# Kernel tuning notes

Hardware: AMD Instinct MI355X
Metric: run time of the kernel (lower is better)

The kernel has to match this reference:

```python
import jax, jax.numpy as jnp
import numpy as np

B, T, C = 4, 2048, 1024   # batch, seq (block_size), n_embd
H, D = 16, 64             # num_heads, head_size (H*D == C)


def setup_inputs() -> dict:
    key = jax.random.key(0)
    ks = jax.random.split(key, 6)
    s = 0.02
    return {
        "x":  jax.random.normal(ks[0], (B, T, C), jnp.float32),
        "Wq": jax.random.normal(ks[1], (H, C, D), jnp.float32) * s,
        "Wk": jax.random.normal(ks[2], (H, C, D), jnp.float32) * s,
        "Wv": jax.random.normal(ks[3], (H, C, D), jnp.float32) * s,
        "Wp": jax.random.normal(ks[4], (C, C), jnp.float32) * s,
        "bp": jnp.zeros((C,), jnp.float32),
        "is_masked": 1,
    }


def reference(x, Wq, Wk, Wv, Wp, bp, is_masked):
    # Batched per-head projections (original loops over H separate Linears)
    q = jnp.einsum("btc,hcd->bhtd", x, Wq)
    k = jnp.einsum("btc,hcd->bhtd", x, Wk)
    v = jnp.einsum("btc,hcd->bhtd", x, Wv)
    # NOTE: original divides by sqrt(C) where C = n_embd (input dim), not head_size
    scores = jnp.einsum("bhtd,bhsd->bhts", q, k) / jnp.sqrt(jnp.asarray(C, x.dtype))
    if is_masked:
        causal = jnp.tril(jnp.ones((T, T), bool))
        scores = jnp.where(causal, scores, jnp.asarray(-jnp.inf, scores.dtype))
    attn = jax.nn.softmax(scores, axis=-1)   # dropout is identity in eval mode
    out = jnp.einsum("bhts,bhsd->bhtd", attn, v)
    # concat heads along the last dim: [B,T,H*D] == [B,T,C]
    out = out.transpose(0, 2, 1, 3).reshape(B, T, C)
    return out @ Wp.T + bp
```

## Files before the change

### kernel.cpp

```cpp
#include <hip/hip_runtime.h>
#include <stdint.h>
#include <type_traits>

typedef unsigned short u16;
typedef unsigned int u32;
typedef __attribute__((ext_vector_type(8))) short frag8;
typedef __attribute__((ext_vector_type(4))) float fx4;
typedef __attribute__((ext_vector_type(16))) float fx16;

#define MFMA(a, b, c) __builtin_amdgcn_mfma_f32_16x16x32_bf16((a), (b), (c), 0, 0, 0)
#define MFMA32(a, b, c) __builtin_amdgcn_mfma_f32_32x32x16_bf16((a), (b), (c), 0, 0, 0)

__device__ __forceinline__ void gload16(const void* g, void* l) {
  __builtin_amdgcn_global_load_lds((const __attribute__((address_space(1))) void*)g,
                                   (__attribute__((address_space(3))) void*)l, 16, 0, 0);
}

__device__ __forceinline__ u16 f2bf(float f) {
  union { float f; unsigned int u; } c; c.f = f;
  unsigned int r = c.u + 0x7FFFu + ((c.u >> 16) & 1u);
  return (u16)(r >> 16);
}

__device__ __forceinline__ u32 cvtpk(float lo, float hi) {
  u32 r;
  asm("v_cvt_pk_bf16_f32 %0, %1, %2" : "=v"(r) : "v"(lo), "v"(hi));
  return r;
}

__device__ __forceinline__ float fmax3(float a, float b, float c) {
  return fmaxf(fmaxf(a, b), c);
}


__global__ __launch_bounds__(256) void cvt_x(const float* __restrict__ x, u16* __restrict__ xb) {
  const int n4 = (8192 * 1024) / 4;
  for (int i = blockIdx.x * 256 + threadIdx.x; i < n4; i += 2048 * 256) {
    float4 v = ((const float4*)x)[i];
    ushort4 o;
    o.x = f2bf(v.x); o.y = f2bf(v.y); o.z = f2bf(v.z); o.w = f2bf(v.w);
    ((ushort4*)xb)[i] = o;
  }
}

__global__ __launch_bounds__(256) void cvt_wqkv(const float* __restrict__ Wq,
                                                const float* __restrict__ Wk,
                                                const float* __restrict__ Wv,
                                                u16* __restrict__ Wt) {
  __shared__ u16 Tls[64][72];
  int hh = blockIdx.x;
  int c0 = blockIdx.y * 64;
  int type = hh >> 4, h = hh & 15;
  const float* Wsrc = (type == 0 ? Wq : (type == 1 ? Wk : Wv)) + (size_t)h * 1024 * 64;
  int t = threadIdx.x;
  int cr = t >> 4, q4 = (t & 15) * 4;
  for (int i = 0; i < 4; ++i) {
    int c = cr + i * 16;
    float4 v = *(const float4*)(Wsrc + (size_t)(c0 + c) * 64 + q4);
    Tls[q4 + 0][c] = f2bf(v.x);
    Tls[q4 + 1][c] = f2bf(v.y);
    Tls[q4 + 2][c] = f2bf(v.z);
    Tls[q4 + 3][c] = f2bf(v.w);
  }
  __syncthreads();
  for (int i = 0; i < 4; ++i) {
    int d = cr + i * 16;
    ushort4 o;
    o.x = Tls[d][q4 + 0]; o.y = Tls[d][q4 + 1]; o.z = Tls[d][q4 + 2]; o.w = Tls[d][q4 + 3];
    *(ushort4*)(Wt + ((size_t)hh * 64 + d) * 1024 + c0 + q4) = o;
  }
}

__global__ __launch_bounds__(256) void cvt_wp(const float* __restrict__ Wp, u16* __restrict__ wb) {
  const int n4 = (1024 * 1024) / 4;
  for (int i = blockIdx.x * 256 + threadIdx.x; i < n4; i += 1024 * 256) {
    float4 v = ((const float4*)Wp)[i];
    ushort4 o;
    o.x = f2bf(v.x); o.y = f2bf(v.y); o.z = f2bf(v.z); o.w = f2bf(v.w);
    ((ushort4*)wb)[i] = o;
  }
}

__global__ __launch_bounds__(256) void transpose_v(const u16* __restrict__ Vb, u16* __restrict__ VTg) {
  __shared__ u16 T[64 * 64];
  int bh = blockIdx.x, t0 = blockIdx.y * 64;
  const u16* src = Vb + ((size_t)bh * 2048 + t0) * 64;
  int tid = threadIdx.x;
  int tl = tid >> 2, c16 = (tid & 3) * 16;
  int swzw = (tl & 7) << 4;
  frag8 a = *(const frag8*)(src + (size_t)tl * 64 + c16);
  frag8 b = *(const frag8*)(src + (size_t)tl * 64 + c16 + 8);
  *(frag8*)((char*)T + tl * 128 + ((c16 * 2) ^ swzw)) = a;
  *(frag8*)((char*)T + tl * 128 + ((c16 * 2 + 16) ^ swzw)) = b;
  __syncthreads();
  int d_ = tid & 63;
#pragma unroll
  for (int k = 0; k < 2; ++k) {
    int c_ = (tid >> 6) + 4 * k;
    frag8 o;
#pragma unroll
    for (int j = 0; j < 8; ++j) {
      int t = c_ * 8 + j;
      o[j] = *(const u16*)((const char*)T + t * 128 + ((2 * d_) ^ ((t & 7) << 4)));
    }
    *(frag8*)(VTg + ((size_t)bh * 64 + d_) * 2048 + t0 + c_ * 8) = o;
  }
}


template <int BN, int MODE>
__global__ __launch_bounds__(512, 1) void gemm2(const u16* __restrict__ A, const u16* __restrict__ Bw,
                                                u16* __restrict__ Qb, u16* __restrict__ Kb,
                                                u16* __restrict__ Vb, float* __restrict__ outp,
                                                const float* __restrict__ bp) {
  constexpr int NI = BN / 32;
  constexpr int NB = BN / 64;
  constexpr int BBYTES = BN * 128;
  __shared__ __align__(16) char LDSC[65536 + 3 * BBYTES];
  const int tid = threadIdx.x, w = tid >> 6, lane = tid & 63;
  const int lr = lane & 15, lg = lane >> 4;
  constexpr int NBY = (BN == 192) ? 16 : 8;
  const int wg = blockIdx.x;
  const int xcd = wg & 7, loc = wg >> 3;
  const int bx = xcd * 4 + loc / NBY;
  const int by = loc % NBY;
  const int m0 = bx * 256, n0 = by * BN;
  const int r8 = lane >> 3;
  const int c8 = ((lane & 7) ^ r8) * 8;
  const u16* aS[4];
  const u16* bS[3];
#pragma unroll
  for (int l = 0; l < 4; ++l) aS[l] = A + (size_t)(m0 + l * 64 + w * 8 + r8) * 1024 + c8;
#pragma unroll
  for (int l = 0; l < NB; ++l) bS[l] = Bw + (size_t)(n0 + l * 64 + w * 8 + r8) * 1024 + c8;
  const int wmB = (w >> 1) * 64, wnB = (w & 1) * (BN / 2);

  auto rdA = [&](const char* ab, int mi, int ks) -> frag8 {
    int row = wmB + mi * 16 + lr;
    return *(const frag8*)(ab + row * 128 + ((((ks << 2) + lg) ^ (lr & 7)) << 4));
  };
  auto rdB = [&](const char* bbuf, int ni, int ks) -> frag8 {
    int row = wnB + ni * 16 + lr;
    return *(const frag8*)(bbuf + row * 128 + ((((ks << 2) + lg) ^ (lr & 7)) << 4));
  };

  fx4 acc[4][NI] = {};

#pragma unroll
  for (int l = 0; l < 4; ++l) gload16(aS[l], LDSC + l * 8192 + w * 1024);
#pragma unroll
  for (int l = 0; l < NB; ++l) gload16(bS[l], LDSC + 65536 + l * 8192 + w * 1024);
#pragma unroll
  for (int l = 0; l < NB; ++l) gload16(bS[l] + 64, LDSC + 65536 + BBYTES + l * 8192 + w * 1024);
  if constexpr (NB == 3) asm volatile("s_waitcnt vmcnt(3)" ::: "memory");
  else asm volatile("s_waitcnt vmcnt(2)" ::: "memory");
  __builtin_amdgcn_s_barrier();

  for (int t = 0; t < 16; ++t) {
    const char* ab = LDSC + (t & 1) * 32768;
    const char* bb = LDSC + 65536 + (t % 3) * BBYTES;
    char* abN = LDSC + ((t + 1) & 1) * 32768;
    char* bbN = LDSC + 65536 + ((t + 2) % 3) * BBYTES;
    if (t + 1 < 16) {
#pragma unroll
      for (int l = 0; l < 4; ++l) gload16(aS[l] + (t + 1) * 64, abN + l * 8192 + w * 1024);
    }
    if (t + 2 < 16) {
#pragma unroll
      for (int l = 0; l < NB; ++l) gload16(bS[l] + (t + 2) * 64, bbN + l * 8192 + w * 1024);
    }
    frag8 Bf[NI][2];
#pragma unroll
    for (int ni = 0; ni < NI; ++ni) {
      Bf[ni][0] = rdB(bb, ni, 0);
      Bf[ni][1] = rdB(bb, ni, 1);
    }
    frag8 a0 = rdA(ab, 0, 0), a1 = rdA(ab, 0, 1);
#pragma unroll
    for (int mi = 0; mi < 4; ++mi) {
      frag8 c0 = a0, c1 = a1;
      if (mi < 3) {
        a0 = rdA(ab, mi + 1, 0);
        a1 = rdA(ab, mi + 1, 1);
      }
      __builtin_amdgcn_s_setprio(1);
#pragma unroll
      for (int ni = 0; ni < NI; ++ni) acc[mi][ni] = MFMA(c0, Bf[ni][0], acc[mi][ni]);
#pragma unroll
      for (int ni = 0; ni < NI; ++ni) acc[mi][ni] = MFMA(c1, Bf[ni][1], acc[mi][ni]);
      __builtin_amdgcn_s_setprio(0);
    }
    if (t < 14) {
      if constexpr (NB == 3) asm volatile("s_waitcnt vmcnt(3)" ::: "memory");
      else asm volatile("s_waitcnt vmcnt(2)" ::: "memory");
    } else {
      asm volatile("s_waitcnt vmcnt(0)" ::: "memory");
    }
    __builtin_amdgcn_s_barrier();
  }

#pragma unroll
  for (int mi = 0; mi < 4; ++mi)
#pragma unroll
    for (int r = 0; r < 4; ++r) {
      int m = m0 + wmB + mi * 16 + lg * 4 + r;
      if (MODE == 0) {
        int b = m >> 11, tt = m & 2047;
#pragma unroll
        for (int ni = 0; ni < NI; ++ni) {
          int n = n0 + wnB + ni * 16 + lr;
          int type = n >> 10, h = (n >> 6) & 15, d = n & 63;
          u16* dst = (type == 0) ? Qb : ((type == 1) ? Kb : Vb);
          float v = acc[mi][ni][r];
          if (type == 0) v *= 0.04508422002778011f;
          dst[((size_t)(b * 16 + h) * 2048 + tt) * 64 + d] = f2bf(v);
        }
      } else {
#pragma unroll
        for (int ni = 0; ni < NI; ++ni) {
          int n = n0 + wnB + ni * 16 + lr;
          outp[(size_t)m * 1024 + n] = acc[mi][ni][r] + bp[n];
        }
      }
    }
}


__global__ __launch_bounds__(256, 4) void attn(const u16* __restrict__ Qb, const u16* __restrict__ Kb,
                                               const u16* __restrict__ VTg, u16* __restrict__ Ao,
                                               const int* __restrict__ mflag) {
  __shared__ __align__(16) char LDS[32768];
  const int tid = threadIdx.x, w = tid >> 6, lane = tid & 63;
  const int l31 = lane & 31, hi = lane >> 5;
  const int bh = blockIdx.x;
  const int qt = 15 - (int)blockIdx.y;
  const int masked = mflag[0];
  const int qbase = qt * 128;
  const u16* Qh = Qb + (size_t)bh * (2048 * 64);
  const u16* Kh = Kb + (size_t)bh * (2048 * 64);
  const u16* Vh = VTg + (size_t)bh * (64 * 2048);
  const int qrow = qbase + w * 32 + l31;
  frag8 qf[4];
#pragma unroll
  for (int s = 0; s < 4; ++s) qf[s] = *(const frag8*)(Qh + (size_t)qrow * 64 + s * 16 + hi * 8);
  const int srow = lane >> 3;
  const int schunk = ((lane & 7) ^ srow) * 8;
  const int c0 = w * 2, c1 = w * 2 + 1;
  const u16* kg0 = Kh + (size_t)(c0 * 8 + srow) * 64 + schunk;
  const u16* kg1 = Kh + (size_t)(c1 * 8 + srow) * 64 + schunk;
  const u16* vg0 = Vh + (size_t)(c0 * 8 + srow) * 2048 + schunk;
  const u16* vg1 = Vh + (size_t)(c1 * 8 + srow) * 2048 + schunk;
  const int aK = l31 * 128 + ((hi * 16) ^ ((l31 & 7) << 4));
  const int qmax_w = qbase + w * 32 + 31;
  const int qmin_w = qbase + w * 32;
  float m_run = -__builtin_inff(), l_run = 0.f;
  fx16 oa0 = {}, oa1 = {};
  const int nt = masked ? (2 * qt + 2) : 32;

  auto STAGE = [&](int B, int T) {
    size_t ko = (size_t)T * 4096, vo = (size_t)T * 64;
    gload16(kg0 + ko, LDS + B * 8192 + c0 * 1024);
    gload16(kg1 + ko, LDS + B * 8192 + c1 * 1024);
    gload16(vg0 + vo, LDS + 16384 + B * 8192 + c0 * 1024);
    gload16(vg1 + vo, LDS + 16384 + B * 8192 + c1 * 1024);
  };

  auto TILE = [&](auto Bc, int T) {
    constexpr int B = decltype(Bc)::value;
    if (T + 1 < nt) STAGE(B ^ 1, T + 1);
    bool act = (!masked) || (T * 64 <= qmax_w);
    if (act) {
      fx16 s0v = {}, s1v = {};
#pragma unroll
      for (int ds = 0; ds < 4; ++ds) {
        frag8 k0 = *(const frag8*)(LDS + B * 8192 + (aK ^ (ds << 5)));
        frag8 k1 = *(const frag8*)(LDS + B * 8192 + 4096 + (aK ^ (ds << 5)));
        s0v = MFMA32(k0, qf[ds], s0v);
        s1v = MFMA32(k1, qf[ds], s1v);
      }
      if (masked && T * 64 + 63 > qmin_w) {
#pragma unroll
        for (int g = 0; g < 4; ++g)
#pragma unroll
          for (int r = 0; r < 4; ++r) {
            int sg = T * 64 + r + 8 * g + 4 * hi;
            if (sg > qrow) s0v[4 * g + r] = -__builtin_inff();
            if (sg + 32 > qrow) s1v[4 * g + r] = -__builtin_inff();
          }
      }
      float tmx[8];
#pragma unroll
      for (int i = 0; i < 8; ++i)
        tmx[i] = fmaxf(fmaxf(s0v[i], s0v[i + 8]), fmaxf(s1v[i], s1v[i + 8]));
      float r0 = fmax3(tmx[0], tmx[1], tmx[2]);
      float r1 = fmax3(tmx[3], tmx[4], tmx[5]);
      float r2 = fmax3(tmx[6], tmx[7], r0);
      float mx = fmaxf(r1, r2);
      mx = fmaxf(mx, __int_as_float(__shfl_xor(__float_as_int(mx), 32)));
      if (!__all(mx <= m_run + 8.0f)) {
        float mn = fmaxf(m_run, mx);
        float al = __builtin_amdgcn_exp2f(m_run - mn);
#pragma unroll
        for (int i = 0; i < 16; ++i) { oa0[i] *= al; oa1[i] *= al; }
        l_run *= al;
        m_run = mn;
      }
#pragma unroll
      for (int i = 0; i < 16; ++i) s0v[i] = __builtin_amdgcn_exp2f(s0v[i] - m_run);
#pragma unroll
      for (int i = 0; i < 16; ++i) s1v[i] = __builtin_amdgcn_exp2f(s1v[i] - m_run);
      float tps[8];
#pragma unroll
      for (int i = 0; i < 8; ++i)
        tps[i] = (s0v[i] + s0v[i + 8]) + (s1v[i] + s1v[i + 8]);
      float u0 = (tps[0] + tps[1]) + (tps[2] + tps[3]);
      float u1 = (tps[4] + tps[5]) + (tps[6] + tps[7]);
      float ps = u0 + u1;
      ps += __int_as_float(__shfl_xor(__float_as_int(ps), 32));
      l_run += ps;
#pragma unroll
      for (int kt = 0; kt < 4; ++kt) {
        const int b8 = (kt & 1) * 8;
        float p0, p1, p2, p3, p4, p5, p6, p7;
        if (kt < 2) { p0=s0v[b8+0];p1=s0v[b8+1];p2=s0v[b8+2];p3=s0v[b8+3];p4=s0v[b8+4];p5=s0v[b8+5];p6=s0v[b8+6];p7=s0v[b8+7]; }
        else        { p0=s1v[b8+0];p1=s1v[b8+1];p2=s1v[b8+2];p3=s1v[b8+3];p4=s1v[b8+4];p5=s1v[b8+5];p6=s1v[b8+6];p7=s1v[b8+7]; }
        u32 X0 = cvtpk(p0, p1), X1 = cvtpk(p2, p3);
        u32 Y0 = cvtpk(p4, p5), Y1 = cvtpk(p6, p7);
        u32 sel0 = hi ? X0 : Y0, sel1 = hi ? X1 : Y1;
        u32 got0 = (u32)__shfl_xor((int)sel0, 32);
        u32 got1 = (u32)__shfl_xor((int)sel1, 32);
        union { u32 u[4]; frag8 f; } pf;
        pf.u[0] = hi ? got0 : X0;
        pf.u[1] = hi ? got1 : X1;
        pf.u[2] = hi ? Y0 : got0;
        pf.u[3] = hi ? Y1 : got1;
        frag8 v0 = *(const frag8*)(LDS + 16384 + B * 8192 + (aK ^ (kt << 5)));
        frag8 v1 = *(const frag8*)(LDS + 16384 + B * 8192 + 4096 + (aK ^ (kt << 5)));
        oa0 = MFMA32(v0, pf.f, oa0);
        oa1 = MFMA32(v1, pf.f, oa1);
      }
    }
    asm volatile("s_waitcnt vmcnt(0)" ::: "memory");
    __builtin_amdgcn_s_barrier();
  };

  STAGE(0, 0);
  asm volatile("s_waitcnt vmcnt(0)" ::: "memory");
  __builtin_amdgcn_s_barrier();
  int t = 0;
  while (true) {
    TILE(std::integral_constant<int, 0>{}, t); ++t; if (t >= nt) break;
    TILE(std::integral_constant<int, 1>{}, t); ++t; if (t >= nt) break;
  }

  float inv = 1.0f / l_run;
  int b = bh >> 4, hh = bh & 15;
  u16* orow = Ao + ((size_t)b * 2048 + qrow) * 1024 + hh * 64;
#pragma unroll
  for (int g = 0; g < 4; ++g) {
    int d0 = 8 * g + 4 * hi;
    u32 wA = cvtpk(oa0[4 * g + 0] * inv, oa0[4 * g + 1] * inv);
    u32 wB = cvtpk(oa0[4 * g + 2] * inv, oa0[4 * g + 3] * inv);
    u32 wC = cvtpk(oa1[4 * g + 0] * inv, oa1[4 * g + 1] * inv);
    u32 wD = cvtpk(oa1[4 * g + 2] * inv, oa1[4 * g + 3] * inv);
    *(u32*)(orow + d0 + 0) = wA;
    *(u32*)(orow + d0 + 2) = wB;
    *(u32*)(orow + d0 + 32) = wC;
    *(u32*)(orow + d0 + 34) = wD;
  }
}


extern "C" void kernel_launch(void* const* d_in, const int* in_sizes, int n_in,
                              void* d_out, int out_size, void* d_ws, size_t ws_size,
                              hipStream_t stream) {
  const float* x = (const float*)d_in[0];
  const float* Wq = (const float*)d_in[1];
  const float* Wk = (const float*)d_in[2];
  const float* Wv = (const float*)d_in[3];
  const float* Wp = (const float*)d_in[4];
  const float* bp = (const float*)d_in[5];
  const int* is_masked = (const int*)d_in[6];
  float* out = (float*)d_out;
  char* ws = (char*)d_ws;
  u16* Xbf = (u16*)(ws + 0);
  u16* Wt  = (u16*)(ws + 16777216);
  u16* Wpb = (u16*)(ws + 23068672);
  u16* Qb  = (u16*)(ws + 25165824);
  u16* Kb  = (u16*)(ws + 41943040);
  u16* Vb  = (u16*)(ws + 58720256);
  u16* Ao  = (u16*)(ws + 75497472);
  u16* VTg = Xbf;

  cvt_x<<<2048, 256, 0, stream>>>(x, Xbf);
  cvt_wqkv<<<dim3(48, 16), 256, 0, stream>>>(Wq, Wk, Wv, Wt);
  cvt_wp<<<1024, 256, 0, stream>>>(Wp, Wpb);
  gemm2<192, 0><<<512, 512, 0, stream>>>(Xbf, Wt, Qb, Kb, Vb, nullptr, nullptr);
  transpose_v<<<dim3(64, 32), 256, 0, stream>>>(Vb, VTg);
  attn<<<dim3(64, 16), 256, 0, stream>>>(Qb, Kb, VTg, Ao, is_masked);
  gemm2<128, 1><<<256, 512, 0, stream>>>(Ao, Wpb, nullptr, nullptr, nullptr, out, bp);
}
```

Baseline: 161.6 us.

## Fuse V transpose into QKV GEMM epilogue and raise MFMA priority in attention

Reorders the QKV weight layout so each 192-column GEMM tile covers the Q, K and V columns of one head. The GEMM epilogue can then write V already transposed, staging it through swizzled LDS. This removes the separate transpose_v kernel launch and its extra round trip of V through global memory. It also wraps the attention MFMA blocks in s_setprio to favour matrix issue, at the cost of an extra LDS pass and a barrier in the GEMM epilogue.

```diff
diff --git a/kernel.cpp b/kernel.cpp
--- a/kernel.cpp
+++ b/kernel.cpp
@@ -67,7 +67,7 @@
     int d = cr + i * 16;
     ushort4 o;
     o.x = Tls[d][q4 + 0]; o.y = Tls[d][q4 + 1]; o.z = Tls[d][q4 + 2]; o.w = Tls[d][q4 + 3];
-    *(ushort4*)(Wt + ((size_t)hh * 64 + d) * 1024 + c0 + q4) = o;
+    *(ushort4*)(Wt + ((size_t)(h * 3 + type) * 64 + d) * 1024 + c0 + q4) = o;
   }
 }
 
@@ -81,37 +81,11 @@
   }
 }
 
-__global__ __launch_bounds__(256) void transpose_v(const u16* __restrict__ Vb, u16* __restrict__ VTg) {
-  __shared__ u16 T[64 * 64];
-  int bh = blockIdx.x, t0 = blockIdx.y * 64;
-  const u16* src = Vb + ((size_t)bh * 2048 + t0) * 64;
-  int tid = threadIdx.x;
-  int tl = tid >> 2, c16 = (tid & 3) * 16;
-  int swzw = (tl & 7) << 4;
-  frag8 a = *(const frag8*)(src + (size_t)tl * 64 + c16);
-  frag8 b = *(const frag8*)(src + (size_t)tl * 64 + c16 + 8);
-  *(frag8*)((char*)T + tl * 128 + ((c16 * 2) ^ swzw)) = a;
-  *(frag8*)((char*)T + tl * 128 + ((c16 * 2 + 16) ^ swzw)) = b;
-  __syncthreads();
-  int d_ = tid & 63;
-#pragma unroll
-  for (int k = 0; k < 2; ++k) {
-    int c_ = (tid >> 6) + 4 * k;
-    frag8 o;
-#pragma unroll
-    for (int j = 0; j < 8; ++j) {
-      int t = c_ * 8 + j;
-      o[j] = *(const u16*)((const char*)T + t * 128 + ((2 * d_) ^ ((t & 7) << 4)));
-    }
-    *(frag8*)(VTg + ((size_t)bh * 64 + d_) * 2048 + t0 + c_ * 8) = o;
-  }
-}
-
 
 template <int BN, int MODE>
 __global__ __launch_bounds__(512, 1) void gemm2(const u16* __restrict__ A, const u16* __restrict__ Bw,
                                                 u16* __restrict__ Qb, u16* __restrict__ Kb,
-                                                u16* __restrict__ Vb, float* __restrict__ outp,
+                                                u16* __restrict__ VTg, float* __restrict__ outp,
                                                 const float* __restrict__ bp) {
   constexpr int NI = BN / 32;
   constexpr int NB = BN / 64;
@@ -199,30 +173,55 @@
     __builtin_amdgcn_s_barrier();
   }
 
-#pragma unroll
-  for (int mi = 0; mi < 4; ++mi)
-#pragma unroll
-    for (int r = 0; r < 4; ++r) {
-      int m = m0 + wmB + mi * 16 + lg * 4 + r;
-      if (MODE == 0) {
-        int b = m >> 11, tt = m & 2047;
+  if constexpr (MODE == 0) {
+    const int b = m0 >> 11, t0b = m0 & 2047;
+    u16* Tls = (u16*)LDSC;
+#pragma unroll
+    for (int mi = 0; mi < 4; ++mi)
+#pragma unroll
+      for (int r = 0; r < 4; ++r) {
+        int row = wmB + mi * 16 + lg * 4 + r;
+        int t = t0b + row;
 #pragma unroll
         for (int ni = 0; ni < NI; ++ni) {
-          int n = n0 + wnB + ni * 16 + lr;
-          int type = n >> 10, h = (n >> 6) & 15, d = n & 63;
-          u16* dst = (type == 0) ? Qb : ((type == 1) ? Kb : Vb);
+          int nl = wnB + ni * 16 + lr;
+          int type = nl >> 6, d = nl & 63;
           float v = acc[mi][ni][r];
-          if (type == 0) v *= 0.04508422002778011f;
-          dst[((size_t)(b * 16 + h) * 2048 + tt) * 64 + d] = f2bf(v);
+          if (type == 0) {
+            v *= 0.04508422002778011f;
+            Qb[((size_t)(b * 16 + by) * 2048 + t) * 64 + d] = f2bf(v);
+          } else if (type == 1) {
+            Kb[((size_t)(b * 16 + by) * 2048 + t) * 64 + d] = f2bf(v);
+          } else {
+            *(u16*)((char*)Tls + d * 512 + ((2 * row) ^ ((d & 7) << 4))) = f2bf(v);
+          }
         }
-      } else {
+      }
+    __syncthreads();
+    {
+      int d = tid >> 3, c = tid & 7;
+      const char* src = (const char*)Tls + d * 512;
+      u16* dst = VTg + ((size_t)(b * 16 + by) * 64 + d) * 2048 + t0b;
+#pragma unroll
+      for (int j = 0; j < 4; ++j) {
+        int o = c * 64 + j * 16;
+        frag8 vv = *(const frag8*)(src + (o ^ ((d & 7) << 4)));
+        *(frag8*)(dst + c * 32 + j * 8) = vv;
+      }
+    }
+  } else {
+#pragma unroll
+    for (int mi = 0; mi < 4; ++mi)
+#pragma unroll
+      for (int r = 0; r < 4; ++r) {
+        int m = m0 + wmB + mi * 16 + lg * 4 + r;
 #pragma unroll
         for (int ni = 0; ni < NI; ++ni) {
           int n = n0 + wnB + ni * 16 + lr;
           outp[(size_t)m * 1024 + n] = acc[mi][ni][r] + bp[n];
         }
       }
-    }
+  }
 }
 
 
@@ -271,6 +270,7 @@
     bool act = (!masked) || (T * 64 <= qmax_w);
     if (act) {
       fx16 s0v = {}, s1v = {};
+      __builtin_amdgcn_s_setprio(1);
 #pragma unroll
       for (int ds = 0; ds < 4; ++ds) {
         frag8 k0 = *(const frag8*)(LDS + B * 8192 + (aK ^ (ds << 5)));
@@ -278,6 +278,7 @@
         s0v = MFMA32(k0, qf[ds], s0v);
         s1v = MFMA32(k1, qf[ds], s1v);
       }
+      __builtin_amdgcn_s_setprio(0);
       if (masked && T * 64 + 63 > qmin_w) {
 #pragma unroll
         for (int g = 0; g < 4; ++g)
@@ -336,8 +337,10 @@
         pf.u[3] = hi ? Y1 : got1;
         frag8 v0 = *(const frag8*)(LDS + 16384 + B * 8192 + (aK ^ (kt << 5)));
         frag8 v1 = *(const frag8*)(LDS + 16384 + B * 8192 + 4096 + (aK ^ (kt << 5)));
+        __builtin_amdgcn_s_setprio(1);
         oa0 = MFMA32(v0, pf.f, oa0);
         oa1 = MFMA32(v1, pf.f, oa1);
+        __builtin_amdgcn_s_setprio(0);
       }
     }
     asm volatile("s_waitcnt vmcnt(0)" ::: "memory");
@@ -388,15 +391,13 @@
   u16* Wpb = (u16*)(ws + 23068672);
   u16* Qb  = (u16*)(ws + 25165824);
   u16* Kb  = (u16*)(ws + 41943040);
-  u16* Vb  = (u16*)(ws + 58720256);
+  u16* VT  = (u16*)(ws + 58720256);
   u16* Ao  = (u16*)(ws + 75497472);
-  u16* VTg = Xbf;
 
   cvt_x<<<2048, 256, 0, stream>>>(x, Xbf);
   cvt_wqkv<<<dim3(48, 16), 256, 0, stream>>>(Wq, Wk, Wv, Wt);
   cvt_wp<<<1024, 256, 0, stream>>>(Wp, Wpb);
-  gemm2<192, 0><<<512, 512, 0, stream>>>(Xbf, Wt, Qb, Kb, Vb, nullptr, nullptr);
-  transpose_v<<<dim3(64, 32), 256, 0, stream>>>(Vb, VTg);
-  attn<<<dim3(64, 16), 256, 0, stream>>>(Qb, Kb, VTg, Ao, is_masked);
+  gemm2<192, 0><<<512, 512, 0, stream>>>(Xbf, Wt, Qb, Kb, VT, nullptr, nullptr);
+  attn<<<dim3(64, 16), 256, 0, stream>>>(Qb, Kb, VT, Ao, is_masked);
   gemm2<128, 1><<<256, 512, 0, stream>>>(Ao, Wpb, nullptr, nullptr, nullptr, out, bp);
 }
```

Result: no change. 159.0 us (-1.6%).
